# Kernel optimization log

Hardware: AMD Instinct MI355X
Metric: run time of the kernel (lower is better)

The kernel has to match this reference:

```python
import jax, jax.numpy as jnp
import numpy as np

IMG_SIZE = 512
NUM_FREQ_MASKS = 4


def _make_masks(n, num):
    # Mirrors DCTTransform._generate_freq_masks: for i in reversed(range(num-1)),
    # an anti-triangular (low-frequency) mask of size n//2**i padded to (n,n),
    # then an all-ones mask appended last.
    masks = []
    for i in reversed(range(num - 1)):
        m = n // (2 ** i)
        tri = np.triu(np.ones((m, m), dtype=np.float32))      # upper triangular
        rot = np.rot90(tri, k=1)                               # -> i+j <= m-1 region
        pad = np.zeros((n, n), dtype=np.float32)
        pad[:m, :m] = rot
        masks.append(pad)
    masks.append(np.ones((n, n), dtype=np.float32))
    return np.stack(masks)  # [num, n, n]


def _dct_matrix(n, dtype=jnp.float32):
    # Orthonormal DCT-II matrix: X = D @ x  ==  scipy.fftpack.dct(x, axis=0, norm='ortho')
    k = jnp.arange(n, dtype=dtype)[:, None]
    m = jnp.arange(n, dtype=dtype)[None, :]
    D = jnp.cos(jnp.pi * (2.0 * m + 1.0) * k / (2.0 * n)) * jnp.sqrt(2.0 / n)
    D = D.at[0].multiply(1.0 / jnp.sqrt(2.0))  # k=0 row scale -> sqrt(1/n)
    return D


def setup_inputs() -> dict:
    key = jax.random.key(0)
    x = jax.random.normal(key, (32, 3, IMG_SIZE, IMG_SIZE), dtype=jnp.float32)
    masks = jnp.asarray(_make_masks(IMG_SIZE, NUM_FREQ_MASKS))
    return {"x": x, "masks": masks}


def reference(x, masks):
    # x: [B, C, H, W] with H == W == img_size; masks: [4, H, W]
    n = x.shape[-1]
    D = _dct_matrix(n, x.dtype)
    # 2D orthonormal DCT-II over last two axes: D @ x @ D^T (separable, order-free)
    dct2 = jnp.einsum('ij,bcjk,lk->bcil', D, x, D)
    outs = []
    for i in range(masks.shape[0]):  # small fixed loop over 4 masks
        masked = dct2 * masks[i]
        # inverse 2D DCT (IDCT-II == DCT-III, orthonormal): D^T @ y @ D
        outs.append(jnp.einsum('ji,bcjk,kl->bcil', D, masked, D))
    LH, HL, HH, LL = outs  # idx 0->LH, 1->HL, 2->HH, 3(ones)->LL per original forward
    return (LL, LH, HL, HH)
```

## Files before the change

### kernel.cpp

```cpp
#include <hip/hip_runtime.h>
#include <hip/hip_bf16.h>
#include <stdint.h>

#define NIMG 96
#define N 512
#define IMG (N*N)
#define OUT_PLANE ((long long)NIMG * IMG)

typedef __attribute__((ext_vector_type(8))) _Float16 f16x8;
typedef __attribute__((ext_vector_type(4))) float f32x4;
typedef unsigned short u16;

__device__ __forceinline__ u16 f2h(float v) {
    _Float16 h = (_Float16)v;
    return __builtin_bit_cast(u16, h);
}

__device__ __forceinline__ void gload16(const void* g, void* l) {
    __builtin_amdgcn_global_load_lds(
        (const __attribute__((address_space(1))) void*)g,
        (__attribute__((address_space(3))) void*)l, 16, 0, 0);
}

__global__ __launch_bounds__(256) void conv_x(const float* __restrict__ x,
                                              u16* __restrict__ Xcm,
                                              float* __restrict__ outLL,
                                              u16* __restrict__ Drm,
                                              u16* __restrict__ Dcm) {
    const int bid = blockIdx.x + (blockIdx.y << 4) + (blockIdx.z << 8);
    if (bid < 1024) {
        int idx = (bid << 8) + threadIdx.x;
        int k = idx >> 9, m = idx & 511;
        int r = ((2 * m + 1) * k) & 2047;
        float c = cospif((float)r * (1.0f / 1024.0f));
        float s = (k == 0) ? 0.04419417382415922f : 0.0625f;
        u16 h = f2h(c * s);
        Drm[(k << 9) + m] = h;
        Dcm[(m << 9) + k] = h;
    }

    __shared__ float t[32][33];
    const long long base = (long long)blockIdx.z * IMG;
    const int r0 = blockIdx.y * 32, c0 = blockIdx.x * 32;
    const int tr = threadIdx.x >> 3;
    const int tc = (threadIdx.x & 7) * 4;
    float4 v = *(const float4*)&x[base + (long long)(r0 + tr) * N + c0 + tc];
    *(float4*)&outLL[base + (long long)(r0 + tr) * N + c0 + tc] = v;
    t[tr][tc + 0] = v.x; t[tr][tc + 1] = v.y;
    t[tr][tc + 2] = v.z; t[tr][tc + 3] = v.w;
    __syncthreads();
    ushort4 h;
    h.x = f2h(t[tc + 0][tr]); h.y = f2h(t[tc + 1][tr]);
    h.z = f2h(t[tc + 2][tr]); h.w = f2h(t[tc + 3][tr]);
    *(ushort4*)&Xcm[base + (long long)(c0 + tr) * N + r0 + tc] = h;
}

#define GEMM_DECLS                                                         \
    const int tid = threadIdx.x;                                           \
    const int wave = tid >> 6;                                             \
    const int lane = tid & 63;                                             \
    const int srow = lane >> 2;                                            \
    const int sc8  = (lane & 3) * 8;                                       \
    const int war  = wave * 32;                                            \
    const int fr   = lane & 15;                                            \
    const int kg8  = (lane >> 4) * 8;                                      \
    const int wr   = (wave >> 1) * 64;                                     \
    const int wc   = (wave & 1) * 64;                                      \
    const int rb   = (lane >> 4) * 4;                                      \
    int aoff[4], boff[4];                                                  \
    _Pragma("unroll")                                                      \
    for (int i = 0; i < 4; ++i) {                                          \
        aoff[i] = (wr + i * 16 + fr) * 32 + kg8;                           \
        boff[i] = (wc + i * 16 + fr) * 32 + kg8;                           \
    }                                                                      \
    f32x4 acc[4][4];                                                       \
    _Pragma("unroll")                                                      \
    for (int i = 0; i < 4; ++i)                                            \
        _Pragma("unroll")                                                  \
        for (int j = 0; j < 4; ++j)                                        \
            acc[i][j] = (f32x4){0.0f, 0.0f, 0.0f, 0.0f};

#define GEMM_LOOP(Ab, lda, Bb, ldb, Keff)                                  \
    {                                                                      \
        auto stage = [&](int buf, int k0) {                                \
            _Pragma("unroll")                                              \
            for (int i = 0; i < 2; ++i) {                                  \
                int r = war + i * 16;                                      \
                gload16((Ab) + (long long)(m0 + r + srow) * (lda) + k0 + sc8, &As[buf][r * 32]); \
                gload16((Bb) + (long long)(n0 + r + srow) * (ldb) + k0 + sc8, &Bs[buf][r * 32]); \
            }                                                              \
        };                                                                 \
        auto compute = [&](int buf) {                                      \
            f16x8 af[4], bf[4];                                            \
            _Pragma("unroll")                                              \
            for (int i = 0; i < 4; ++i) af[i] = *(const f16x8*)&As[buf][aoff[i]]; \
            _Pragma("unroll")                                              \
            for (int j = 0; j < 4; ++j) bf[j] = *(const f16x8*)&Bs[buf][boff[j]]; \
            _Pragma("unroll")                                              \
            for (int i = 0; i < 4; ++i)                                    \
                _Pragma("unroll")                                          \
                for (int j = 0; j < 4; ++j)                                \
                    acc[i][j] = __builtin_amdgcn_mfma_f32_16x16x32_f16(af[i], bf[j], acc[i][j], 0, 0, 0); \
        };                                                                 \
        const int nb = (Keff) >> 5;                                        \
        stage(0, 0);                                                       \
        __syncthreads();                                                   \
        int cur = 0;                                                       \
        for (int t = 0; t < nb - 1; ++t) {                                 \
            stage(cur ^ 1, (t + 1) * 32);                                  \
            compute(cur);                                                  \
            __syncthreads();                                               \
            cur ^= 1;                                                      \
        }                                                                  \
        compute(cur);                                                      \
    }

template<int EPI>
__global__ __launch_bounds__(256) void gemm16(
    const u16* __restrict__ A, long long sA, int lda,
    const u16* __restrict__ B, long long sB, int ldb,
    void* __restrict__ Cv, long long sC, int ldc,
    int K, int trilim,
    u16* __restrict__ Y2, u16* __restrict__ Y3)
{
    __shared__ u16 As[2][128 * 32];
    __shared__ u16 Bs[2][128 * 32];
    const int bz = blockIdx.z;
    const int m0 = blockIdx.y * 128;
    const int n0 = blockIdx.x * 128;

    if (EPI == 3 && (m0 + n0 > trilim)) return;

    const u16* __restrict__ Ab = A + (long long)bz * sA;
    const u16* __restrict__ Bb = B + (long long)bz * sB;

    GEMM_DECLS
    GEMM_LOOP(Ab, lda, Bb, ldb, K)

    if (EPI == 0) {
        float* Cb = (float*)Cv + (long long)bz * sC;
        #pragma unroll
        for (int i = 0; i < 4; ++i)
            #pragma unroll
            for (int j = 0; j < 4; ++j) {
                int r = m0 + wr + i * 16 + rb;
                int c = n0 + wc + j * 16 + fr;
                #pragma unroll
                for (int g = 0; g < 4; ++g)
                    Cb[(long long)(r + g) * ldc + c] = acc[i][j][g];
            }
    } else if (EPI == 1) {
        u16* Cb = (u16*)Cv + (long long)bz * sC;
        #pragma unroll
        for (int i = 0; i < 4; ++i)
            #pragma unroll
            for (int j = 0; j < 4; ++j) {
                int r = m0 + wr + i * 16 + rb;
                int c = n0 + wc + j * 16 + fr;
                #pragma unroll
                for (int g = 0; g < 4; ++g)
                    Cb[(long long)(r + g) * ldc + c] = f2h(acc[i][j][g]);
            }
    } else {
        u16* Cb = (u16*)Cv + (long long)bz * sC;
        u16* Y2b = Y2 + (long long)bz * (256 * 256);
        u16* Y3b = Y3 + (long long)bz * (128 * 128);
        const bool doY2 = (m0 + n0 < 256);
        #pragma unroll
        for (int i = 0; i < 4; ++i)
            #pragma unroll
            for (int j = 0; j < 4; ++j) {
                int r = m0 + wr + i * 16 + rb;
                int c = n0 + wc + j * 16 + fr;
                float v0 = ((r + 0) + c <= trilim) ? acc[i][j][0] : 0.0f;
                float v1 = ((r + 1) + c <= trilim) ? acc[i][j][1] : 0.0f;
                float v2 = ((r + 2) + c <= trilim) ? acc[i][j][2] : 0.0f;
                float v3 = ((r + 3) + c <= trilim) ? acc[i][j][3] : 0.0f;
                ushort4 h;
                h.x = f2h(v0); h.y = f2h(v1); h.z = f2h(v2); h.w = f2h(v3);
                *(ushort4*)&Cb[(long long)c * ldc + r] = h;
                if (doY2 && r < 256 && c < 256) {
                    ushort4 h2;
                    h2.x = ((r + 0) + c <= 255) ? h.x : (u16)0;
                    h2.y = ((r + 1) + c <= 255) ? h.y : (u16)0;
                    h2.z = ((r + 2) + c <= 255) ? h.z : (u16)0;
                    h2.w = ((r + 3) + c <= 255) ? h.w : (u16)0;
                    *(ushort4*)&Y2b[(long long)c * 256 + r] = h2;
                }
                if (r < 128 && c < 128) {
                    ushort4 h3;
                    h3.x = ((r + 0) + c <= 127) ? h.x : (u16)0;
                    h3.y = ((r + 1) + c <= 127) ? h.y : (u16)0;
                    h3.z = ((r + 2) + c <= 127) ? h.z : (u16)0;
                    h3.w = ((r + 3) + c <= 127) ? h.w : (u16)0;
                    *(ushort4*)&Y3b[(long long)c * 128 + r] = h3;
                }
            }
    }
}

__global__ __launch_bounds__(256) void invA(
    const u16* __restrict__ Ycm, const u16* __restrict__ Y2,
    const u16* __restrict__ Y3, const u16* __restrict__ Dcm,
    u16* __restrict__ U, u16* __restrict__ U2, u16* __restrict__ U3)
{
    __shared__ u16 As[2][128 * 32];
    __shared__ u16 Bs[2][128 * 32];
    const int bz = blockIdx.z;
    const int id = blockIdx.x;

    const u16* __restrict__ Ab;
    u16* __restrict__ Cb;
    int lda, ldc, Keff, m0, n0;
    if (id < 16) {
        m0 = (id >> 2) * 128; n0 = (id & 3) * 128;
        Ab = Ycm + (long long)bz * IMG;     lda = 512;
        Cb = U   + (long long)bz * IMG;     ldc = 512;
        Keff = 512 - m0;
    } else if (id < 24) {
        int t = id - 16;
        m0 = (t >> 2) * 128; n0 = (t & 3) * 128;
        Ab = Y2 + (long long)bz * 65536;    lda = 256;
        Cb = U2 + (long long)bz * 131072;   ldc = 256;
        Keff = 256 - m0;
    } else {
        int t = id - 24;
        m0 = 0;              n0 = (t & 3) * 128;
        Ab = Y3 + (long long)bz * 16384;    lda = 128;
        Cb = U3 + (long long)bz * 65536;    ldc = 128;
        Keff = 128;
    }
    const u16* __restrict__ Bb = Dcm;
    const int ldb = 512;

    GEMM_DECLS
    GEMM_LOOP(Ab, lda, Bb, ldb, Keff)

    #pragma unroll
    for (int i = 0; i < 4; ++i)
        #pragma unroll
        for (int j = 0; j < 4; ++j) {
            int r = m0 + wr + i * 16 + rb;
            int c = n0 + wc + j * 16 + fr;
            ushort4 h;
            h.x = f2h(acc[i][j][0]); h.y = f2h(acc[i][j][1]);
            h.z = f2h(acc[i][j][2]); h.w = f2h(acc[i][j][3]);
            *(ushort4*)&Cb[(long long)c * ldc + r] = h;
        }
}

__global__ __launch_bounds__(256) void invC(
    const u16* __restrict__ U2, const u16* __restrict__ U3,
    const u16* __restrict__ U, const u16* __restrict__ Dcm,
    float* __restrict__ outHL, float* __restrict__ outLH,
    float* __restrict__ outHH)
{
    __shared__ u16 As[2][128 * 32];
    __shared__ u16 Bs[2][128 * 32];
    const int bz = blockIdx.z;
    const int id = blockIdx.x;

    const u16* __restrict__ Ab;
    float* __restrict__ Cb;
    int lda, Keff, m0, n0;
    if (id < 16) {
        m0 = (id >> 2) * 128; n0 = (id & 3) * 128;
        Ab = U2 + (long long)bz * 131072;  lda = 256; Keff = 256;
        Cb = outHL + (long long)bz * IMG;
    } else if (id < 32) {
        int t = id - 16;
        m0 = (t >> 2) * 128; n0 = (t & 3) * 128;
        Ab = U3 + (long long)bz * 65536;   lda = 128; Keff = 128;
        Cb = outLH + (long long)bz * IMG;
    } else {
        int t = id - 32;
        m0 = (t >> 2) * 128; n0 = (t & 3) * 128;
        Ab = U + (long long)bz * IMG;      lda = 512; Keff = 512;
        Cb = outHH + (long long)bz * IMG;
    }
    const u16* __restrict__ Bb = Dcm;
    const int ldb = 512;
    const int ldc = 512;

    GEMM_DECLS
    GEMM_LOOP(Ab, lda, Bb, ldb, Keff)

    #pragma unroll
    for (int i = 0; i < 4; ++i)
        #pragma unroll
        for (int j = 0; j < 4; ++j) {
            int r = m0 + wr + i * 16 + rb;
            int c = n0 + wc + j * 16 + fr;
            #pragma unroll
            for (int g = 0; g < 4; ++g)
                Cb[(long long)(r + g) * ldc + c] = acc[i][j][g];
        }
}

extern "C" void kernel_launch(void* const* d_in, const int* in_sizes, int n_in,
                              void* d_out, int out_size, void* d_ws, size_t ws_size,
                              hipStream_t stream) {
    const float* x = (const float*)d_in[0];
    float* out = (float*)d_out;
    float* outLL = out + 0 * OUT_PLANE;
    float* outLH = out + 1 * OUT_PLANE;
    float* outHL = out + 2 * OUT_PLANE;
    float* outHH = out + 3 * OUT_PLANE;

    char* ws = (char*)d_ws;
    u16* Drm = (u16*)(ws);
    u16* Dcm = (u16*)(ws + 524288);
    u16* Xcm = (u16*)(ws + 1048576);
    u16* Ycm = Xcm;
    char* reg = ws + 51380224;
    u16* T1 = (u16*)reg;
    u16* U  = (u16*)reg;
    u16* Y2 = (u16*)(ws + 101711872);
    u16* Y3 = (u16*)(ws + 114294784);
    u16* U2 = (u16*)(ws + 117440512);
    u16* U3 = (u16*)(ws + 142606336);

    const long long S = IMG;
    const int BIG = 1 << 30;

    conv_x<<<dim3(16, 16, NIMG), 256, 0, stream>>>(x, Xcm, outLL, Drm, Dcm);

    gemm16<1><<<dim3(4, 4, NIMG), 256, 0, stream>>>(
        Drm, 0, 512, Xcm, S, 512, T1, S, 512, 512, BIG, nullptr, nullptr);
    gemm16<3><<<dim3(4, 4, NIMG), 256, 0, stream>>>(
        T1, S, 512, Drm, 0, 512, Ycm, S, 512, 512, 511, Y2, Y3);
    invA<<<dim3(28, 1, NIMG), 256, 0, stream>>>(Ycm, Y2, Y3, Dcm, U, U2, U3);
    invC<<<dim3(48, 1, NIMG), 256, 0, stream>>>(U2, U3, U, Dcm, outHL, outLH, outHH);
}
```

Before: 343.7 us.

## Use DCT even/odd symmetry to halve GEMM work in forward and inverse stages

Splits the DCT matrix into even and odd rows and folds the input as x[i]±x[511-i], so each 512-length DCT becomes two 256-length GEMMs. This applies to the forward row and column transforms and to the first inverse stage, with new fold kernels recombining the half results. The aim is to cut the MFMA FLOPs of those GEMMs roughly in half. In exchange it adds extra elementwise kernels and intermediate buffer traffic, and the butterfly sums are done in fp16, which can cost accuracy.

```diff
diff --git a/kernel.cpp b/kernel.cpp
--- a/kernel.cpp
+++ b/kernel.cpp
@@ -22,12 +22,17 @@
         (__attribute__((address_space(3))) void*)l, 16, 0, 0);
 }
 
-__global__ __launch_bounds__(256) void conv_x(const float* __restrict__ x,
-                                              u16* __restrict__ Xcm,
-                                              float* __restrict__ outLL,
-                                              u16* __restrict__ Drm,
-                                              u16* __restrict__ Dcm) {
-    const int bid = blockIdx.x + (blockIdx.y << 4) + (blockIdx.z << 8);
+
+__global__ __launch_bounds__(256) void convF(const float* __restrict__ x,
+                                             u16* __restrict__ Xp,
+                                             u16* __restrict__ Xm,
+                                             float* __restrict__ outLL,
+                                             u16* __restrict__ Dcm,
+                                             u16* __restrict__ De,
+                                             u16* __restrict__ Do_,
+                                             u16* __restrict__ DeT,
+                                             u16* __restrict__ DoT) {
+    const int bid = blockIdx.x + (blockIdx.y << 4) + (blockIdx.z << 7);
     if (bid < 1024) {
         int idx = (bid << 8) + threadIdx.x;
         int k = idx >> 9, m = idx & 511;
@@ -35,24 +40,36 @@
         float c = cospif((float)r * (1.0f / 1024.0f));
         float s = (k == 0) ? 0.04419417382415922f : 0.0625f;
         u16 h = f2h(c * s);
-        Drm[(k << 9) + m] = h;
         Dcm[(m << 9) + k] = h;
+        if (m < 256) {
+            int kh = k >> 1;
+            if ((k & 1) == 0) { De[(kh << 8) + m] = h;  DeT[(m << 8) + kh] = h; }
+            else              { Do_[(kh << 8) + m] = h; DoT[(m << 8) + kh] = h; }
+        }
     }
 
-    __shared__ float t[32][33];
+    __shared__ float sP[32][33], sM[32][33];
     const long long base = (long long)blockIdx.z * IMG;
     const int r0 = blockIdx.y * 32, c0 = blockIdx.x * 32;
     const int tr = threadIdx.x >> 3;
     const int tc = (threadIdx.x & 7) * 4;
-    float4 v = *(const float4*)&x[base + (long long)(r0 + tr) * N + c0 + tc];
-    *(float4*)&outLL[base + (long long)(r0 + tr) * N + c0 + tc] = v;
-    t[tr][tc + 0] = v.x; t[tr][tc + 1] = v.y;
-    t[tr][tc + 2] = v.z; t[tr][tc + 3] = v.w;
+    float4 a = *(const float4*)&x[base + (long long)(r0 + tr) * N + c0 + tc];
+    float4 b = *(const float4*)&x[base + (long long)(511 - r0 - tr) * N + c0 + tc];
+    *(float4*)&outLL[base + (long long)(r0 + tr) * N + c0 + tc] = a;
+    *(float4*)&outLL[base + (long long)(511 - r0 - tr) * N + c0 + tc] = b;
+    sP[tr][tc + 0] = a.x + b.x; sP[tr][tc + 1] = a.y + b.y;
+    sP[tr][tc + 2] = a.z + b.z; sP[tr][tc + 3] = a.w + b.w;
+    sM[tr][tc + 0] = a.x - b.x; sM[tr][tc + 1] = a.y - b.y;
+    sM[tr][tc + 2] = a.z - b.z; sM[tr][tc + 3] = a.w - b.w;
     __syncthreads();
-    ushort4 h;
-    h.x = f2h(t[tc + 0][tr]); h.y = f2h(t[tc + 1][tr]);
-    h.z = f2h(t[tc + 2][tr]); h.w = f2h(t[tc + 3][tr]);
-    *(ushort4*)&Xcm[base + (long long)(c0 + tr) * N + r0 + tc] = h;
+    ushort4 hp, hm;
+    hp.x = f2h(sP[tc + 0][tr]); hp.y = f2h(sP[tc + 1][tr]);
+    hp.z = f2h(sP[tc + 2][tr]); hp.w = f2h(sP[tc + 3][tr]);
+    hm.x = f2h(sM[tc + 0][tr]); hm.y = f2h(sM[tc + 1][tr]);
+    hm.z = f2h(sM[tc + 2][tr]); hm.w = f2h(sM[tc + 3][tr]);
+    const long long pb = (long long)blockIdx.z * 131072;
+    *(ushort4*)&Xp[pb + (long long)(c0 + tr) * 256 + r0 + tc] = hp;
+    *(ushort4*)&Xm[pb + (long long)(c0 + tr) * 256 + r0 + tc] = hm;
 }
 
 #define GEMM_DECLS                                                         \
@@ -115,138 +132,209 @@
         compute(cur);                                                      \
     }
 
-template<int EPI>
-__global__ __launch_bounds__(256) void gemm16(
-    const u16* __restrict__ A, long long sA, int lda,
-    const u16* __restrict__ B, long long sB, int ldb,
-    void* __restrict__ Cv, long long sC, int ldc,
-    int K, int trilim,
-    u16* __restrict__ Y2, u16* __restrict__ Y3)
-{
-    __shared__ u16 As[2][128 * 32];
-    __shared__ u16 Bs[2][128 * 32];
-    const int bz = blockIdx.z;
-    const int m0 = blockIdx.y * 128;
-    const int n0 = blockIdx.x * 128;
-
-    if (EPI == 3 && (m0 + n0 > trilim)) return;
-
-    const u16* __restrict__ Ab = A + (long long)bz * sA;
-    const u16* __restrict__ Bb = B + (long long)bz * sB;
-
-    GEMM_DECLS
-    GEMM_LOOP(Ab, lda, Bb, ldb, K)
-
-    if (EPI == 0) {
-        float* Cb = (float*)Cv + (long long)bz * sC;
-        #pragma unroll
-        for (int i = 0; i < 4; ++i)
-            #pragma unroll
-            for (int j = 0; j < 4; ++j) {
-                int r = m0 + wr + i * 16 + rb;
-                int c = n0 + wc + j * 16 + fr;
-                #pragma unroll
-                for (int g = 0; g < 4; ++g)
-                    Cb[(long long)(r + g) * ldc + c] = acc[i][j][g];
-            }
-    } else if (EPI == 1) {
-        u16* Cb = (u16*)Cv + (long long)bz * sC;
-        #pragma unroll
-        for (int i = 0; i < 4; ++i)
-            #pragma unroll
-            for (int j = 0; j < 4; ++j) {
-                int r = m0 + wr + i * 16 + rb;
-                int c = n0 + wc + j * 16 + fr;
-                #pragma unroll
-                for (int g = 0; g < 4; ++g)
-                    Cb[(long long)(r + g) * ldc + c] = f2h(acc[i][j][g]);
-            }
-    } else {
-        u16* Cb = (u16*)Cv + (long long)bz * sC;
-        u16* Y2b = Y2 + (long long)bz * (256 * 256);
-        u16* Y3b = Y3 + (long long)bz * (128 * 128);
-        const bool doY2 = (m0 + n0 < 256);
-        #pragma unroll
-        for (int i = 0; i < 4; ++i)
-            #pragma unroll
-            for (int j = 0; j < 4; ++j) {
-                int r = m0 + wr + i * 16 + rb;
-                int c = n0 + wc + j * 16 + fr;
-                float v0 = ((r + 0) + c <= trilim) ? acc[i][j][0] : 0.0f;
-                float v1 = ((r + 1) + c <= trilim) ? acc[i][j][1] : 0.0f;
-                float v2 = ((r + 2) + c <= trilim) ? acc[i][j][2] : 0.0f;
-                float v3 = ((r + 3) + c <= trilim) ? acc[i][j][3] : 0.0f;
-                ushort4 h;
-                h.x = f2h(v0); h.y = f2h(v1); h.z = f2h(v2); h.w = f2h(v3);
-                *(ushort4*)&Cb[(long long)c * ldc + r] = h;
-                if (doY2 && r < 256 && c < 256) {
-                    ushort4 h2;
-                    h2.x = ((r + 0) + c <= 255) ? h.x : (u16)0;
-                    h2.y = ((r + 1) + c <= 255) ? h.y : (u16)0;
-                    h2.z = ((r + 2) + c <= 255) ? h.z : (u16)0;
-                    h2.w = ((r + 3) + c <= 255) ? h.w : (u16)0;
-                    *(ushort4*)&Y2b[(long long)c * 256 + r] = h2;
-                }
-                if (r < 128 && c < 128) {
-                    ushort4 h3;
-                    h3.x = ((r + 0) + c <= 127) ? h.x : (u16)0;
-                    h3.y = ((r + 1) + c <= 127) ? h.y : (u16)0;
-                    h3.z = ((r + 2) + c <= 127) ? h.z : (u16)0;
-                    h3.w = ((r + 3) + c <= 127) ? h.w : (u16)0;
-                    *(ushort4*)&Y3b[(long long)c * 128 + r] = h3;
-                }
-            }
-    }
-}
-
-__global__ __launch_bounds__(256) void invA(
-    const u16* __restrict__ Ycm, const u16* __restrict__ Y2,
-    const u16* __restrict__ Y3, const u16* __restrict__ Dcm,
-    u16* __restrict__ U, u16* __restrict__ U2, u16* __restrict__ U3)
+#define EPI_F16_RM(Cb, ldc)                                                \
+    _Pragma("unroll")                                                      \
+    for (int i = 0; i < 4; ++i)                                            \
+        _Pragma("unroll")                                                  \
+        for (int j = 0; j < 4; ++j) {                                      \
+            int r = m0 + wr + i * 16 + rb;                                 \
+            int c = n0 + wc + j * 16 + fr;                                 \
+            _Pragma("unroll")                                              \
+            for (int g = 0; g < 4; ++g)                                    \
+                (Cb)[(long long)(r + g) * (ldc) + c] = f2h(acc[i][j][g]);  \
+        }
+
+__global__ __launch_bounds__(256) void gemmF1(
+    const u16* __restrict__ De, const u16* __restrict__ Do_,
+    const u16* __restrict__ Xp, const u16* __restrict__ Xm,
+    u16* __restrict__ T1e, u16* __restrict__ T1o)
 {
     __shared__ u16 As[2][128 * 32];
     __shared__ u16 Bs[2][128 * 32];
     const int bz = blockIdx.z;
     const int id = blockIdx.x;
-
-    const u16* __restrict__ Ab;
-    u16* __restrict__ Cb;
-    int lda, ldc, Keff, m0, n0;
-    if (id < 16) {
-        m0 = (id >> 2) * 128; n0 = (id & 3) * 128;
-        Ab = Ycm + (long long)bz * IMG;     lda = 512;
-        Cb = U   + (long long)bz * IMG;     ldc = 512;
-        Keff = 512 - m0;
-    } else if (id < 24) {
-        int t = id - 16;
-        m0 = (t >> 2) * 128; n0 = (t & 3) * 128;
-        Ab = Y2 + (long long)bz * 65536;    lda = 256;
-        Cb = U2 + (long long)bz * 131072;   ldc = 256;
-        Keff = 256 - m0;
-    } else {
-        int t = id - 24;
-        m0 = 0;              n0 = (t & 3) * 128;
-        Ab = Y3 + (long long)bz * 16384;    lda = 128;
-        Cb = U3 + (long long)bz * 65536;    ldc = 128;
-        Keff = 128;
-    }
-    const u16* __restrict__ Bb = Dcm;
-    const int ldb = 512;
+    const int p = id >> 3, sub = id & 7;
+    const int m0 = ((sub >> 2) & 1) * 128;
+    const int n0 = (sub & 3) * 128;
+    const u16* __restrict__ Ab = p ? Do_ : De;
+    const u16* __restrict__ Bb = (p ? Xm : Xp) + (long long)bz * 131072;
+    u16* __restrict__ Cb = (p ? T1o : T1e) + (long long)bz * 131072;
 
     GEMM_DECLS
-    GEMM_LOOP(Ab, lda, Bb, ldb, Keff)
-
+    GEMM_LOOP(Ab, 256, Bb, 256, 256)
+    EPI_F16_RM(Cb, 512)
+}
+
+__global__ __launch_bounds__(256) void foldT1(
+    const u16* __restrict__ T1e, const u16* __restrict__ T1o,
+    u16* __restrict__ T1p, u16* __restrict__ T1m)
+{
+    int t = blockIdx.x * 256 + threadIdx.x;
+    int img = t >> 14;
+    int rem = t & 16383;
+    int p = rem >> 13;
+    int k = (rem >> 5) & 255;
+    int j0 = (rem & 31) * 8;
+    const u16* src = (p ? T1o : T1e) + (long long)img * 131072 + k * 512;
+    f16x8 a = *(const f16x8*)&src[j0];
+    f16x8 b = *(const f16x8*)&src[504 - j0];
+    f16x8 br = __builtin_shufflevector(b, b, 7, 6, 5, 4, 3, 2, 1, 0);
+    f16x8 s = a + br;
+    f16x8 d = a - br;
+    long long dst = (long long)img * 131072 + (long long)(2 * k + p) * 256 + j0;
+    *(f16x8*)&T1p[dst] = s;
+    *(f16x8*)&T1m[dst] = d;
+}
+
+__global__ __launch_bounds__(256) void gemmF2(
+    const u16* __restrict__ T1p, const u16* __restrict__ T1m,
+    const u16* __restrict__ De, const u16* __restrict__ Do_,
+    u16* __restrict__ YRe, u16* __restrict__ YRo,
+    u16* __restrict__ Y2Re, u16* __restrict__ Y2Ro,
+    u16* __restrict__ Y3Re, u16* __restrict__ Y3Ro)
+{
+    __shared__ u16 As[2][128 * 32];
+    __shared__ u16 Bs[2][128 * 32];
+    const int bz = blockIdx.z;
+    const int id = blockIdx.x;
+    const int p = id >> 3, sub = id & 7;
+    const int m0 = (sub >> 1) * 128;
+    const int n0 = (sub & 1) * 128;
+    if (m0 + 2 * n0 > 511) return;
+
+    const u16* __restrict__ Ab = (p ? T1m : T1p) + (long long)bz * 131072;
+    const u16* __restrict__ Bb = p ? Do_ : De;
+
+    GEMM_DECLS
+    GEMM_LOOP(Ab, 256, Bb, 256, 256)
+
+    u16* YReb = YRe + (long long)bz * 131072;
+    u16* YRob = YRo + (long long)bz * 131072;
+    u16* Y2Reb = Y2Re + (long long)bz * 32768;
+    u16* Y2Rob = Y2Ro + (long long)bz * 32768;
+    u16* Y3Reb = Y3Re + (long long)bz * 8192;
+    u16* Y3Rob = Y3Ro + (long long)bz * 8192;
     #pragma unroll
     for (int i = 0; i < 4; ++i)
         #pragma unroll
         for (int j = 0; j < 4; ++j) {
             int r = m0 + wr + i * 16 + rb;
             int c = n0 + wc + j * 16 + fr;
-            ushort4 h;
-            h.x = f2h(acc[i][j][0]); h.y = f2h(acc[i][j][1]);
-            h.z = f2h(acc[i][j][2]); h.w = f2h(acc[i][j][3]);
-            *(ushort4*)&Cb[(long long)c * ldc + r] = h;
+            int l = 2 * c + p;
+            float v0 = ((r + 0) + l <= 511) ? acc[i][j][0] : 0.0f;
+            float v1 = ((r + 1) + l <= 511) ? acc[i][j][1] : 0.0f;
+            float v2 = ((r + 2) + l <= 511) ? acc[i][j][2] : 0.0f;
+            float v3 = ((r + 3) + l <= 511) ? acc[i][j][3] : 0.0f;
+            u16 h0 = f2h(v0), h1 = f2h(v1), h2 = f2h(v2), h3 = f2h(v3);
+            ushort2 he; he.x = h0; he.y = h2;
+            ushort2 ho; ho.x = h1; ho.y = h3;
+            *(ushort2*)&YReb[(long long)l * 256 + (r >> 1)] = he;
+            *(ushort2*)&YRob[(long long)l * 256 + (r >> 1)] = ho;
+            if (r < 256 && l < 256) {
+                ushort2 h2e, h2o;
+                h2e.x = ((r + 0) + l <= 255) ? h0 : (u16)0;
+                h2e.y = ((r + 2) + l <= 255) ? h2 : (u16)0;
+                h2o.x = ((r + 1) + l <= 255) ? h1 : (u16)0;
+                h2o.y = ((r + 3) + l <= 255) ? h3 : (u16)0;
+                *(ushort2*)&Y2Reb[(long long)l * 128 + (r >> 1)] = h2e;
+                *(ushort2*)&Y2Rob[(long long)l * 128 + (r >> 1)] = h2o;
+            }
+            if (r < 128 && l < 128) {
+                ushort2 h3e, h3o;
+                h3e.x = ((r + 0) + l <= 127) ? h0 : (u16)0;
+                h3e.y = ((r + 2) + l <= 127) ? h2 : (u16)0;
+                h3o.x = ((r + 1) + l <= 127) ? h1 : (u16)0;
+                h3o.y = ((r + 3) + l <= 127) ? h3 : (u16)0;
+                *(ushort2*)&Y3Reb[(long long)l * 64 + (r >> 1)] = h3e;
+                *(ushort2*)&Y3Rob[(long long)l * 64 + (r >> 1)] = h3o;
+            }
         }
+}
+
+__global__ __launch_bounds__(256) void invAf(
+    const u16* __restrict__ DeT, const u16* __restrict__ DoT,
+    const u16* __restrict__ YRe, const u16* __restrict__ YRo,
+    const u16* __restrict__ Y2Re, const u16* __restrict__ Y2Ro,
+    const u16* __restrict__ Y3Re, const u16* __restrict__ Y3Ro,
+    u16* __restrict__ Ue, u16* __restrict__ Uo,
+    u16* __restrict__ U2e, u16* __restrict__ U2o,
+    u16* __restrict__ U3e, u16* __restrict__ U3o)
+{
+    __shared__ u16 As[2][128 * 32];
+    __shared__ u16 Bs[2][128 * 32];
+    const int bz = blockIdx.z;
+    const int id = blockIdx.x;
+
+    const u16* __restrict__ Ab;
+    const u16* __restrict__ Bb;
+    u16* __restrict__ Cb;
+    int ldb, ldc, Keff, m0, n0;
+    if (id < 16) {
+        int p = (id >> 3) & 1, sub = id & 7;
+        m0 = ((sub >> 2) & 1) * 128; n0 = (sub & 3) * 128;
+        Ab = p ? DoT : DeT;
+        Bb = (p ? YRo : YRe) + (long long)bz * 131072;  ldb = 256;
+        Cb = (p ? Uo : Ue) + (long long)bz * 131072;    ldc = 512;
+        Keff = (512 - n0) >> 1;
+    } else if (id < 24) {
+        int t = id - 16;
+        int p = t >> 2, sub = t & 3;
+        m0 = ((sub >> 1) & 1) * 128; n0 = (sub & 1) * 128;
+        Ab = p ? DoT : DeT;
+        Bb = (p ? Y2Ro : Y2Re) + (long long)bz * 32768; ldb = 128;
+        Cb = (p ? U2o : U2e) + (long long)bz * 65536;   ldc = 256;
+        Keff = n0 ? 64 : 128;
+    } else {
+        int t = id - 24;
+        int p = t >> 1;
+        m0 = (t & 1) * 128; n0 = 0;
+        Ab = p ? DoT : DeT;
+        Bb = (p ? Y3Ro : Y3Re) + (long long)bz * 8192;  ldb = 64;
+        Cb = (p ? U3o : U3e) + (long long)bz * 32768;   ldc = 128;
+        Keff = 64;
+    }
+
+    GEMM_DECLS
+    GEMM_LOOP(Ab, 256, Bb, ldb, Keff)
+    EPI_F16_RM(Cb, ldc)
+}
+
+__global__ __launch_bounds__(256) void foldUs(
+    const u16* __restrict__ Ue, const u16* __restrict__ Uo,
+    const u16* __restrict__ U2e, const u16* __restrict__ U2o,
+    const u16* __restrict__ U3e, const u16* __restrict__ U3o,
+    u16* __restrict__ U, u16* __restrict__ U2, u16* __restrict__ U3)
+{
+    int t = blockIdx.x * 256 + threadIdx.x;
+    int img = t / 28672;
+    int rem = t % 28672;
+    if (rem < 16384) {
+        int m = rem >> 6, j0 = (rem & 63) * 8;
+        long long s = (long long)img * 131072 + (long long)m * 512 + j0;
+        f16x8 a = *(const f16x8*)&Ue[s];
+        f16x8 b = *(const f16x8*)&Uo[s];
+        long long dbase = (long long)img * 262144;
+        *(f16x8*)&U[dbase + (long long)m * 512 + j0] = a + b;
+        *(f16x8*)&U[dbase + (long long)(511 - m) * 512 + j0] = a - b;
+    } else if (rem < 24576) {
+        int r2 = rem - 16384;
+        int m = r2 >> 5, j0 = (r2 & 31) * 8;
+        long long s = (long long)img * 65536 + (long long)m * 256 + j0;
+        f16x8 a = *(const f16x8*)&U2e[s];
+        f16x8 b = *(const f16x8*)&U2o[s];
+        long long dbase = (long long)img * 131072;
+        *(f16x8*)&U2[dbase + (long long)m * 256 + j0] = a + b;
+        *(f16x8*)&U2[dbase + (long long)(511 - m) * 256 + j0] = a - b;
+    } else {
+        int r3 = rem - 24576;
+        int m = r3 >> 4, j0 = (r3 & 15) * 8;
+        long long s = (long long)img * 32768 + (long long)m * 128 + j0;
+        f16x8 a = *(const f16x8*)&U3e[s];
+        f16x8 b = *(const f16x8*)&U3o[s];
+        long long dbase = (long long)img * 65536;
+        *(f16x8*)&U3[dbase + (long long)m * 128 + j0] = a + b;
+        *(f16x8*)&U3[dbase + (long long)(511 - m) * 128 + j0] = a - b;
+    }
 }
 
 __global__ __launch_bounds__(256) void invC(
@@ -308,27 +396,42 @@
     float* outHH = out + 3 * OUT_PLANE;
 
     char* ws = (char*)d_ws;
-    u16* Drm = (u16*)(ws);
-    u16* Dcm = (u16*)(ws + 524288);
-    u16* Xcm = (u16*)(ws + 1048576);
-    u16* Ycm = Xcm;
-    char* reg = ws + 51380224;
-    u16* T1 = (u16*)reg;
-    u16* U  = (u16*)reg;
-    u16* Y2 = (u16*)(ws + 101711872);
-    u16* Y3 = (u16*)(ws + 114294784);
-    u16* U2 = (u16*)(ws + 117440512);
-    u16* U3 = (u16*)(ws + 142606336);
-
-    const long long S = IMG;
-    const int BIG = 1 << 30;
-
-    conv_x<<<dim3(16, 16, NIMG), 256, 0, stream>>>(x, Xcm, outLL, Drm, Dcm);
-
-    gemm16<1><<<dim3(4, 4, NIMG), 256, 0, stream>>>(
-        Drm, 0, 512, Xcm, S, 512, T1, S, 512, 512, BIG, nullptr, nullptr);
-    gemm16<3><<<dim3(4, 4, NIMG), 256, 0, stream>>>(
-        T1, S, 512, Drm, 0, 512, Ycm, S, 512, 512, 511, Y2, Y3);
-    invA<<<dim3(28, 1, NIMG), 256, 0, stream>>>(Ycm, Y2, Y3, Dcm, U, U2, U3);
+    u16* Dcm = (u16*)(ws);
+    u16* De  = (u16*)(ws + 524288);
+    u16* Do_ = (u16*)(ws + 655360);
+    u16* DeT = (u16*)(ws + 786432);
+    u16* DoT = (u16*)(ws + 917504);
+    u16* Xp  = (u16*)(ws + 1048576);
+    u16* Xm  = (u16*)(ws + 26214400);
+    u16* T1p = Xp;
+    u16* T1m = Xm;
+    u16* U   = (u16*)(ws + 1048576);
+    u16* T1e = (u16*)(ws + 51380224);
+    u16* T1o = (u16*)(ws + 76546048);
+    u16* Ue  = T1e;
+    u16* Uo  = T1o;
+    u16* YRe = (u16*)(ws + 101711872);
+    u16* YRo = (u16*)(ws + 126877696);
+    u16* U2  = YRe;
+    u16* U3  = YRo;
+    u16* Y2Re = (u16*)(ws + 152043520);
+    u16* Y2Ro = (u16*)(ws + 158334976);
+    u16* Y3Re = (u16*)(ws + 164626432);
+    u16* Y3Ro = (u16*)(ws + 166199296);
+    u16* U2e  = (u16*)(ws + 167772160);
+    u16* U2o  = (u16*)(ws + 180355072);
+    u16* U3e  = (u16*)(ws + 192937984);
+    u16* U3o  = (u16*)(ws + 199229440);
+
+    convF<<<dim3(16, 8, NIMG), 256, 0, stream>>>(x, Xp, Xm, outLL,
+                                                 Dcm, De, Do_, DeT, DoT);
+    gemmF1<<<dim3(16, 1, NIMG), 256, 0, stream>>>(De, Do_, Xp, Xm, T1e, T1o);
+    foldT1<<<dim3(6144), 256, 0, stream>>>(T1e, T1o, T1p, T1m);
+    gemmF2<<<dim3(16, 1, NIMG), 256, 0, stream>>>(T1p, T1m, De, Do_,
+                                                  YRe, YRo, Y2Re, Y2Ro, Y3Re, Y3Ro);
+    invAf<<<dim3(28, 1, NIMG), 256, 0, stream>>>(DeT, DoT, YRe, YRo,
+                                                 Y2Re, Y2Ro, Y3Re, Y3Ro,
+                                                 Ue, Uo, U2e, U2o, U3e, U3o);
+    foldUs<<<dim3(10752), 256, 0, stream>>>(Ue, Uo, U2e, U2o, U3e, U3o, U, U2, U3);
     invC<<<dim3(48, 1, NIMG), 256, 0, stream>>>(U2, U3, U, Dcm, outHL, outLH, outHH);
 }
```

Measured after the change: 359.1 us. 4.5% more time.
